# Optimization experiments

Hardware: AMD Instinct MI355X
Metric: run time of the kernel (lower is better)

Reference implementation:

```python
import jax, jax.numpy as jnp
import numpy as np

NUM_STEPS = 50  # fixed-step Dormand-Prince (5th-order) integrator steps

# Dormand-Prince (DOPRI5) Butcher tableau (6 stages needed for the 5th-order solution)
A21 = 1/5
A31, A32 = 3/40, 9/40
A41, A42, A43 = 44/45, -56/15, 32/9
A51, A52, A53, A54 = 19372/6561, -25360/2187, 64448/6561, -212/729
A61, A62, A63, A64, A65 = 9017/3168, -355/33, 46732/5247, 49/176, -5103/18656
B1, B3, B4, B5, B6 = 35/384, 500/1113, 125/192, -2187/6784, 11/84


def setup_inputs() -> dict:
    key = jax.random.key(0)
    ks = jax.random.split(key, 6)
    shape = (2048, 2048)
    f32 = jnp.float32
    re_z = 0.5 * jax.random.normal(ks[0], shape, dtype=f32)
    im_z = 0.5 * jax.random.normal(ks[1], shape, dtype=f32)
    re_a = 0.2 * jax.random.normal(ks[2], shape, dtype=f32)   # small linear growth rate
    im_a = jax.random.normal(ks[3], shape, dtype=f32)          # rotation frequency
    re_b = jax.random.uniform(ks[4], shape, dtype=f32) + 0.1   # positive -> stable limit cycle
    im_b = 0.5 * jax.random.normal(ks[5], shape, dtype=f32)
    return {"re_z": re_z, "im_z": im_z, "re_a": re_a, "im_a": im_a,
            "re_b": re_b, "im_b": im_b, "stp": 0, "unts": 16}


def reference(re_z, im_z, re_a, im_a, re_b, im_b, stp, unts):
    # Hopf normal form: dz/dt = (a - b * conj(z) * z) * z, integrated t in [0, 2pi - 2pi/unts]
    z0 = jax.lax.complex(re_z, im_z)
    a = jax.lax.complex(re_a, im_a)
    b = jax.lax.complex(re_b, im_b)
    t1 = 2.0 * np.pi - 2.0 * np.pi / float(unts)
    h = jnp.float32(t1 / NUM_STEPS)

    def f(z):
        return (a - b * (jnp.conj(z) * z)) * z

    def step(z, _):
        k1 = f(z)
        k2 = f(z + h * (A21 * k1))
        k3 = f(z + h * (A31 * k1 + A32 * k2))
        k4 = f(z + h * (A41 * k1 + A42 * k2 + A43 * k3))
        k5 = f(z + h * (A51 * k1 + A52 * k2 + A53 * k3 + A54 * k4))
        k6 = f(z + h * (A61 * k1 + A62 * k2 + A63 * k3 + A64 * k4 + A65 * k5))
        z_new = z + h * (B1 * k1 + B3 * k3 + B4 * k4 + B5 * k5 + B6 * k6)
        return z_new, None

    zf, _ = jax.lax.scan(step, z0, None, length=NUM_STEPS)
    # return real/imag stacked (original returns complex z_t)
    return jnp.stack([jnp.real(zf), jnp.imag(zf)])
```

## Files before the change

### kernel.cpp

```cpp
#include <hip/hip_runtime.h>
#include <math.h>

#define NUM_STEPS 50

__device__ __forceinline__ void feval(float ar, float ai, float br, float bi,
                                      float zr, float zi,
                                      float& kr, float& ki)
{
    float m  = fmaf(zi, zi, zr * zr);
    float cr = fmaf(-br, m, ar);
    float ci = fmaf(-bi, m, ai);
    kr = fmaf(cr, zr, -(ci * zi));
    ki = fmaf(cr, zi,  (ci * zr));
}

__global__ __launch_bounds__(256) void hopf_dopri5_kernel(
    const float* __restrict__ re_z, const float* __restrict__ im_z,
    const float* __restrict__ re_a, const float* __restrict__ im_a,
    const float* __restrict__ re_b, const float* __restrict__ im_b,
    const int*  __restrict__ unts_p,
    float* __restrict__ out, int n)
{
    const int t = blockIdx.x * blockDim.x + threadIdx.x;
    const int i = t * 2;
    if (i >= n) return;

    const int unts = unts_p[0];
    const double t1 = 2.0 * M_PI - 2.0 * M_PI / (double)unts;
    const float h = (float)(t1 / (double)NUM_STEPS);

    const float hA21 = h * (float)(1.0/5.0);
    const float hA31 = h * (float)(3.0/40.0),      hA32 = h * (float)(9.0/40.0);
    const float hA41 = h * (float)(44.0/45.0),     hA42 = h * (float)(-56.0/15.0),
                hA43 = h * (float)(32.0/9.0);
    const float hA51 = h * (float)(19372.0/6561.0),  hA52 = h * (float)(-25360.0/2187.0),
                hA53 = h * (float)(64448.0/6561.0),  hA54 = h * (float)(-212.0/729.0);
    const float hA61 = h * (float)(9017.0/3168.0),   hA62 = h * (float)(-355.0/33.0),
                hA63 = h * (float)(46732.0/5247.0),  hA64 = h * (float)(49.0/176.0),
                hA65 = h * (float)(-5103.0/18656.0);
    const float hB1  = h * (float)(35.0/384.0),      hB3  = h * (float)(500.0/1113.0),
                hB4  = h * (float)(125.0/192.0),     hB5  = h * (float)(-2187.0/6784.0),
                hB6  = h * (float)(11.0/84.0);

    const float2 zr2 = *(const float2*)(re_z + i);
    const float2 zi2 = *(const float2*)(im_z + i);
    const float2 ar2 = *(const float2*)(re_a + i);
    const float2 ai2 = *(const float2*)(im_a + i);
    const float2 br2 = *(const float2*)(re_b + i);
    const float2 bi2 = *(const float2*)(im_b + i);

    float zr[2] = {zr2.x, zr2.y};
    float zi[2] = {zi2.x, zi2.y};
    const float ar[2] = {ar2.x, ar2.y};
    const float ai[2] = {ai2.x, ai2.y};
    const float br[2] = {br2.x, br2.y};
    const float bi[2] = {bi2.x, bi2.y};

    for (int s = 0; s < NUM_STEPS; ++s) {
        #pragma unroll
        for (int u = 0; u < 2; ++u) {
            float k1r,k1i,k2r,k2i,k3r,k3i,k4r,k4i,k5r,k5i,k6r,k6i;
            float tr, ti;
            const float Ar = ar[u], Ai = ai[u], Br = br[u], Bi = bi[u];
            float Zr = zr[u], Zi = zi[u];

            feval(Ar,Ai,Br,Bi, Zr,Zi, k1r,k1i);

            tr = fmaf(hA21,k1r, Zr);
            ti = fmaf(hA21,k1i, Zi);
            feval(Ar,Ai,Br,Bi, tr,ti, k2r,k2i);

            tr = fmaf(hA31,k1r, fmaf(hA32,k2r, Zr));
            ti = fmaf(hA31,k1i, fmaf(hA32,k2i, Zi));
            feval(Ar,Ai,Br,Bi, tr,ti, k3r,k3i);

            tr = fmaf(hA41,k1r, fmaf(hA42,k2r, fmaf(hA43,k3r, Zr)));
            ti = fmaf(hA41,k1i, fmaf(hA42,k2i, fmaf(hA43,k3i, Zi)));
            feval(Ar,Ai,Br,Bi, tr,ti, k4r,k4i);

            tr = fmaf(hA51,k1r, fmaf(hA52,k2r, fmaf(hA53,k3r, fmaf(hA54,k4r, Zr))));
            ti = fmaf(hA51,k1i, fmaf(hA52,k2i, fmaf(hA53,k3i, fmaf(hA54,k4i, Zi))));
            feval(Ar,Ai,Br,Bi, tr,ti, k5r,k5i);

            tr = fmaf(hA61,k1r, fmaf(hA62,k2r, fmaf(hA63,k3r, fmaf(hA64,k4r, fmaf(hA65,k5r, Zr)))));
            ti = fmaf(hA61,k1i, fmaf(hA62,k2i, fmaf(hA63,k3i, fmaf(hA64,k4i, fmaf(hA65,k5i, Zi)))));
            feval(Ar,Ai,Br,Bi, tr,ti, k6r,k6i);

            zr[u] = fmaf(hB1,k1r, fmaf(hB3,k3r, fmaf(hB4,k4r, fmaf(hB5,k5r, fmaf(hB6,k6r, Zr)))));
            zi[u] = fmaf(hB1,k1i, fmaf(hB3,k3i, fmaf(hB4,k4i, fmaf(hB5,k5i, fmaf(hB6,k6i, Zi)))));
        }
    }

    *(float2*)(out + i)     = make_float2(zr[0], zr[1]);
    *(float2*)(out + n + i) = make_float2(zi[0], zi[1]);
}

extern "C" void kernel_launch(void* const* d_in, const int* in_sizes, int n_in,
                              void* d_out, int out_size, void* d_ws, size_t ws_size,
                              hipStream_t stream) {
    const float* re_z = (const float*)d_in[0];
    const float* im_z = (const float*)d_in[1];
    const float* re_a = (const float*)d_in[2];
    const float* im_a = (const float*)d_in[3];
    const float* re_b = (const float*)d_in[4];
    const float* im_b = (const float*)d_in[5];
    const int*   unts = (const int*)d_in[7];
    float* out = (float*)d_out;

    const int n = in_sizes[0];
    const int threads = (n + 1) / 2;
    const int block = 256;
    const int grid = (threads + block - 1) / block;

    hopf_dopri5_kernel<<<grid, block, 0, stream>>>(re_z, im_z, re_a, im_a,
                                                   re_b, im_b, unts, out, n);
}
```

Measured before the change: 451.1 us.

## Process four elements per thread and keep step coefficients in scalar registers

Each thread now integrates four elements using float4 loads and stores instead of two, which halves the thread count and exposes more independent instruction streams for latency hiding. The 20 h-scaled Butcher coefficients are forced into scalar registers with readfirstlane, which frees vector registers, and the time-step loop is explicitly not unrolled. The trade-off is fewer waves in flight, with 1M threads across the device and longer per-thread serial work, plus higher per-thread register pressure from four live states.

```diff
diff --git a/kernel.cpp b/kernel.cpp
--- a/kernel.cpp
+++ b/kernel.cpp
@@ -3,16 +3,18 @@
 
 #define NUM_STEPS 50
 
-__device__ __forceinline__ void feval(float ar, float ai, float br, float bi,
-                                      float zr, float zi,
-                                      float& kr, float& ki)
-{
-    float m  = fmaf(zi, zi, zr * zr);
-    float cr = fmaf(-br, m, ar);
-    float ci = fmaf(-bi, m, ai);
-    kr = fmaf(cr, zr, -(ci * zi));
-    ki = fmaf(cr, zi,  (ci * zr));
+__device__ __forceinline__ float sbc(float x) {
+    return __int_as_float(__builtin_amdgcn_readfirstlane(__float_as_int(x)));
 }
+
+#define FEVAL(ZR, ZI, KR, KI, AR, AI, BR, BI)            \
+    {                                                    \
+        float m_  = fmaf((ZI), (ZI), (ZR) * (ZR));       \
+        float cr_ = fmaf(-(BR), m_, (AR));               \
+        float ci_ = fmaf(-(BI), m_, (AI));               \
+        (KR) = fmaf(cr_, (ZR), -(ci_ * (ZI)));           \
+        (KI) = fmaf(cr_, (ZI),  (ci_ * (ZR)));           \
+    }
 
 __global__ __launch_bounds__(256) void hopf_dopri5_kernel(
     const float* __restrict__ re_z, const float* __restrict__ im_z,
@@ -22,77 +24,77 @@
     float* __restrict__ out, int n)
 {
     const int t = blockIdx.x * blockDim.x + threadIdx.x;
-    const int i = t * 2;
+    const int i = t * 4;
     if (i >= n) return;
 
     const int unts = unts_p[0];
     const double t1 = 2.0 * M_PI - 2.0 * M_PI / (double)unts;
-    const float h = (float)(t1 / (double)NUM_STEPS);
+    const float h = sbc((float)(t1 / (double)NUM_STEPS));
 
-    const float hA21 = h * (float)(1.0/5.0);
-    const float hA31 = h * (float)(3.0/40.0),      hA32 = h * (float)(9.0/40.0);
-    const float hA41 = h * (float)(44.0/45.0),     hA42 = h * (float)(-56.0/15.0),
-                hA43 = h * (float)(32.0/9.0);
-    const float hA51 = h * (float)(19372.0/6561.0),  hA52 = h * (float)(-25360.0/2187.0),
-                hA53 = h * (float)(64448.0/6561.0),  hA54 = h * (float)(-212.0/729.0);
-    const float hA61 = h * (float)(9017.0/3168.0),   hA62 = h * (float)(-355.0/33.0),
-                hA63 = h * (float)(46732.0/5247.0),  hA64 = h * (float)(49.0/176.0),
-                hA65 = h * (float)(-5103.0/18656.0);
-    const float hB1  = h * (float)(35.0/384.0),      hB3  = h * (float)(500.0/1113.0),
-                hB4  = h * (float)(125.0/192.0),     hB5  = h * (float)(-2187.0/6784.0),
-                hB6  = h * (float)(11.0/84.0);
+    const float hA21 = sbc(h * (float)(1.0/5.0));
+    const float hA31 = sbc(h * (float)(3.0/40.0));
+    const float hA32 = sbc(h * (float)(9.0/40.0));
+    const float hA41 = sbc(h * (float)(44.0/45.0));
+    const float hA42 = sbc(h * (float)(-56.0/15.0));
+    const float hA43 = sbc(h * (float)(32.0/9.0));
+    const float hA51 = sbc(h * (float)(19372.0/6561.0));
+    const float hA52 = sbc(h * (float)(-25360.0/2187.0));
+    const float hA53 = sbc(h * (float)(64448.0/6561.0));
+    const float hA54 = sbc(h * (float)(-212.0/729.0));
+    const float hA61 = sbc(h * (float)(9017.0/3168.0));
+    const float hA62 = sbc(h * (float)(-355.0/33.0));
+    const float hA63 = sbc(h * (float)(46732.0/5247.0));
+    const float hA64 = sbc(h * (float)(49.0/176.0));
+    const float hA65 = sbc(h * (float)(-5103.0/18656.0));
+    const float hB1  = sbc(h * (float)(35.0/384.0));
+    const float hB3  = sbc(h * (float)(500.0/1113.0));
+    const float hB4  = sbc(h * (float)(125.0/192.0));
+    const float hB5  = sbc(h * (float)(-2187.0/6784.0));
+    const float hB6  = sbc(h * (float)(11.0/84.0));
 
-    const float2 zr2 = *(const float2*)(re_z + i);
-    const float2 zi2 = *(const float2*)(im_z + i);
-    const float2 ar2 = *(const float2*)(re_a + i);
-    const float2 ai2 = *(const float2*)(im_a + i);
-    const float2 br2 = *(const float2*)(re_b + i);
-    const float2 bi2 = *(const float2*)(im_b + i);
+    const float4 zr4 = *(const float4*)(re_z + i);
+    const float4 zi4 = *(const float4*)(im_z + i);
+    const float4 ar4 = *(const float4*)(re_a + i);
+    const float4 ai4 = *(const float4*)(im_a + i);
+    const float4 br4 = *(const float4*)(re_b + i);
+    const float4 bi4 = *(const float4*)(im_b + i);
 
-    float zr[2] = {zr2.x, zr2.y};
-    float zi[2] = {zi2.x, zi2.y};
-    const float ar[2] = {ar2.x, ar2.y};
-    const float ai[2] = {ai2.x, ai2.y};
-    const float br[2] = {br2.x, br2.y};
-    const float bi[2] = {bi2.x, bi2.y};
+    float z0r = zr4.x, z1r = zr4.y, z2r = zr4.z, z3r = zr4.w;
+    float z0i = zi4.x, z1i = zi4.y, z2i = zi4.z, z3i = zi4.w;
 
+    #pragma unroll 1
     for (int s = 0; s < NUM_STEPS; ++s) {
-        #pragma unroll
-        for (int u = 0; u < 2; ++u) {
-            float k1r,k1i,k2r,k2i,k3r,k3i,k4r,k4i,k5r,k5i,k6r,k6i;
-            float tr, ti;
-            const float Ar = ar[u], Ai = ai[u], Br = br[u], Bi = bi[u];
-            float Zr = zr[u], Zi = zi[u];
-
-            feval(Ar,Ai,Br,Bi, Zr,Zi, k1r,k1i);
-
-            tr = fmaf(hA21,k1r, Zr);
-            ti = fmaf(hA21,k1i, Zi);
-            feval(Ar,Ai,Br,Bi, tr,ti, k2r,k2i);
-
-            tr = fmaf(hA31,k1r, fmaf(hA32,k2r, Zr));
-            ti = fmaf(hA31,k1i, fmaf(hA32,k2i, Zi));
-            feval(Ar,Ai,Br,Bi, tr,ti, k3r,k3i);
-
-            tr = fmaf(hA41,k1r, fmaf(hA42,k2r, fmaf(hA43,k3r, Zr)));
-            ti = fmaf(hA41,k1i, fmaf(hA42,k2i, fmaf(hA43,k3i, Zi)));
-            feval(Ar,Ai,Br,Bi, tr,ti, k4r,k4i);
-
-            tr = fmaf(hA51,k1r, fmaf(hA52,k2r, fmaf(hA53,k3r, fmaf(hA54,k4r, Zr))));
-            ti = fmaf(hA51,k1i, fmaf(hA52,k2i, fmaf(hA53,k3i, fmaf(hA54,k4i, Zi))));
-            feval(Ar,Ai,Br,Bi, tr,ti, k5r,k5i);
-
-            tr = fmaf(hA61,k1r, fmaf(hA62,k2r, fmaf(hA63,k3r, fmaf(hA64,k4r, fmaf(hA65,k5r, Zr)))));
-            ti = fmaf(hA61,k1i, fmaf(hA62,k2i, fmaf(hA63,k3i, fmaf(hA64,k4i, fmaf(hA65,k5i, Zi)))));
-            feval(Ar,Ai,Br,Bi, tr,ti, k6r,k6i);
-
-            zr[u] = fmaf(hB1,k1r, fmaf(hB3,k3r, fmaf(hB4,k4r, fmaf(hB5,k5r, fmaf(hB6,k6r, Zr)))));
-            zi[u] = fmaf(hB1,k1i, fmaf(hB3,k3i, fmaf(hB4,k4i, fmaf(hB5,k5i, fmaf(hB6,k6i, Zi)))));
+#define STEP(ZR, ZI, AR, AI, BR, BI)                                            \
+        {                                                                       \
+            float k1r,k1i,k2r,k2i,k3r,k3i,k4r,k4i,k5r,k5i,k6r,k6i,tr,ti;        \
+            FEVAL(ZR, ZI, k1r, k1i, AR, AI, BR, BI)                             \
+            tr = fmaf(hA21,k1r, ZR);                                            \
+            ti = fmaf(hA21,k1i, ZI);                                            \
+            FEVAL(tr, ti, k2r, k2i, AR, AI, BR, BI)                             \
+            tr = fmaf(hA31,k1r, fmaf(hA32,k2r, ZR));                            \
+            ti = fmaf(hA31,k1i, fmaf(hA32,k2i, ZI));                            \
+            FEVAL(tr, ti, k3r, k3i, AR, AI, BR, BI)                             \
+            tr = fmaf(hA41,k1r, fmaf(hA42,k2r, fmaf(hA43,k3r, ZR)));            \
+            ti = fmaf(hA41,k1i, fmaf(hA42,k2i, fmaf(hA43,k3i, ZI)));            \
+            FEVAL(tr, ti, k4r, k4i, AR, AI, BR, BI)                             \
+            tr = fmaf(hA51,k1r, fmaf(hA52,k2r, fmaf(hA53,k3r, fmaf(hA54,k4r, ZR)))); \
+            ti = fmaf(hA51,k1i, fmaf(hA52,k2i, fmaf(hA53,k3i, fmaf(hA54,k4i, ZI)))); \
+            FEVAL(tr, ti, k5r, k5i, AR, AI, BR, BI)                             \
+            tr = fmaf(hA61,k1r, fmaf(hA62,k2r, fmaf(hA63,k3r, fmaf(hA64,k4r, fmaf(hA65,k5r, ZR))))); \
+            ti = fmaf(hA61,k1i, fmaf(hA62,k2i, fmaf(hA63,k3i, fmaf(hA64,k4i, fmaf(hA65,k5i, ZI))))); \
+            FEVAL(tr, ti, k6r, k6i, AR, AI, BR, BI)                             \
+            ZR = fmaf(hB1,k1r, fmaf(hB3,k3r, fmaf(hB4,k4r, fmaf(hB5,k5r, fmaf(hB6,k6r, ZR))))); \
+            ZI = fmaf(hB1,k1i, fmaf(hB3,k3i, fmaf(hB4,k4i, fmaf(hB5,k5i, fmaf(hB6,k6i, ZI))))); \
         }
+        STEP(z0r, z0i, ar4.x, ai4.x, br4.x, bi4.x)
+        STEP(z1r, z1i, ar4.y, ai4.y, br4.y, bi4.y)
+        STEP(z2r, z2i, ar4.z, ai4.z, br4.z, bi4.z)
+        STEP(z3r, z3i, ar4.w, ai4.w, br4.w, bi4.w)
+#undef STEP
     }
 
-    *(float2*)(out + i)     = make_float2(zr[0], zr[1]);
-    *(float2*)(out + n + i) = make_float2(zi[0], zi[1]);
+    *(float4*)(out + i)     = make_float4(z0r, z1r, z2r, z3r);
+    *(float4*)(out + n + i) = make_float4(z0i, z1i, z2i, z3i);
 }
 
 extern "C" void kernel_launch(void* const* d_in, const int* in_sizes, int n_in,
@@ -108,7 +110,7 @@
     float* out = (float*)d_out;
 
     const int n = in_sizes[0];
-    const int threads = (n + 1) / 2;
+    const int threads = (n + 3) / 4;
     const int block = 256;
     const int grid = (threads + block - 1) / block;
 
```

After: 464.6 us. 1.03x slower.
